# Performance work log

Measured on AMD Instinct MI355X. Metric: run time of the kernel, lower is better.

Reference implementation:

```python
import jax, jax.numpy as jnp
import numpy as np

B, L, E, H, D = 4, 4096, 1024, 16, 64  # batch, seq, embed, heads, head_dim
EPS = 1e-6


def setup_inputs() -> dict:
    key = jax.random.key(0)
    k1, k2, k3 = jax.random.split(key, 3)
    return {
        "q": jax.random.normal(k1, (B, L, E), dtype=jnp.float32),
        "k": jax.random.normal(k2, (B, L, E), dtype=jnp.float32),
        "v": jax.random.normal(k3, (B, L, E), dtype=jnp.float32),
        "mask": jnp.ones((B, L), dtype=jnp.float32),
    }


def _split_heads(x):
    # (B, L, E) -> (B*H, L, D)
    return x.reshape(B, L, H, D).transpose(0, 2, 1, 3).reshape(B * H, L, D)


def reference(q, k, v, mask):
    # feature map: relu
    q = jax.nn.relu(q)
    k = jax.nn.relu(k)
    # padding mask applied to keys/values
    k = k * mask[:, :, None]
    v = v * mask[:, :, None]
    q = _split_heads(q)
    k = _split_heads(k)
    v = _split_heads(v)
    # cosFormer sin/cos reweighting: pi/2 * i / m for i = 1..L
    idx = (np.pi / 2) * jnp.arange(1, L + 1, dtype=jnp.float32) / L
    s = jnp.sin(idx)[None, :, None]  # (1, L, 1)
    c = jnp.cos(idx)[None, :, None]
    q_ = jnp.concatenate([q * s, q * c], axis=-1)  # (B*H, L, 2D)
    k_ = jnp.concatenate([k * s, k * c], axis=-1)
    # linear-attention KV accumulation (non-causal): (B*H, 2D, D)
    kv = jnp.einsum('nld,nlm->ndm', k_, v)
    # normalizer
    z = 1.0 / jnp.maximum(jnp.einsum('nld,nd->nl', q_, k_.sum(axis=1)), EPS)
    out = jnp.einsum('nld,ndm,nl->nlm', q_, kv, z)  # (B*H, L, D)
    return out.reshape(B, H, L, D)
```

## Files before the change

### kernel.cpp

```cpp
#include <hip/hip_runtime.h>
#include <hip/hip_bf16.h>
#include <math.h>

#define B_ 4
#define L_ 4096
#define E_ 1024
#define H_ 16
#define D_ 64
#define N_ 64
#define D2_ 128
#define EPS_ 1e-6f

#define CH_ 16
#define LC_ (L_ / CH_)
#define LT_ 64

typedef short short8 __attribute__((ext_vector_type(8)));
typedef float f32x4 __attribute__((ext_vector_type(4)));
typedef unsigned int u32;
typedef unsigned short u16;

static __device__ __forceinline__ u32 pack2bf(float a, float b) {
  union { __hip_bfloat16 h; u16 s; } x, y;
  x.h = __float2bfloat16(a);
  y.h = __float2bfloat16(b);
  return (u32)x.s | ((u32)y.s << 16);
}

__global__ __launch_bounds__(256, 4) void phase1_mfma(
    const float* __restrict__ k, const float* __restrict__ v,
    const float* __restrict__ mask,
    float* __restrict__ part_kv, float* __restrict__ part_ks) {
  __shared__ __align__(16) u16 ka[D2_ * 72];
  __shared__ __align__(16) u16 vt[D_ * 72];
  __shared__ float msh[LT_], ssh[LT_], csh[LT_];

  const int bid = blockIdx.x;
  const int n = bid & 63;
  const int ch = bid >> 6;
  const int b = n >> 4;
  const int h = n & 15;
  const int t = threadIdx.x;
  const int wv = t >> 6;
  const int lane = t & 63;
  const int c_lo = lane & 15;
  const int lp = lane >> 4;
  const int c = wv * 16 + c_lo;

  f32x4 acc[2][4];
#pragma unroll
  for (int i = 0; i < 2; ++i)
#pragma unroll
    for (int j = 0; j < 4; ++j) acc[i][j] = (f32x4)0.f;
  float kss = 0.f, ksc = 0.f;

  const float angscale = 0.5f * 3.14159265358979f / (float)L_;

  for (int st = 0; st < LC_ / LT_; ++st) {
    const int l0 = ch * LC_ + st * LT_;
    __syncthreads();
    if (t < LT_) {
      const int gl = l0 + t;
      msh[t] = mask[b * L_ + gl];
      const float ang = (float)(gl + 1) * angscale;
      ssh[t] = __sinf(ang);
      csh[t] = __cosf(ang);
    }
    __syncthreads();
#pragma unroll
    for (int i = 0; i < 8; ++i) {
      const int l = 8 * i + 2 * lp;
      const size_t g0 = (size_t)(b * L_ + l0 + l) * E_ + h * 64 + c;
      const float k0 = k[g0], k1 = k[g0 + E_];
      const float v0 = v[g0], v1 = v[g0 + E_];
      const float m0 = msh[l], m1 = msh[l + 1];
      const float s0 = ssh[l], s1 = ssh[l + 1];
      const float c0 = csh[l], c1 = csh[l + 1];
      const float kr0 = fmaxf(k0, 0.f) * m0;
      const float kr1 = fmaxf(k1, 0.f) * m1;
      const float ks0 = kr0 * s0, ks1 = kr1 * s1;
      const float kc0 = kr0 * c0, kc1 = kr1 * c1;
      const int li = l >> 1;
      ((u32*)ka)[c * 36 + li]        = pack2bf(ks0, ks1);
      ((u32*)ka)[(c + 64) * 36 + li] = pack2bf(kc0, kc1);
      ((u32*)vt)[c * 36 + li]        = pack2bf(v0 * m0, v1 * m1);
      kss += ks0 + ks1;
      ksc += kc0 + kc1;
    }
    __syncthreads();
#pragma unroll
    for (int kk = 0; kk < 2; ++kk) {
      const int colo = kk * 32 + lp * 8;
      short8 af[2], bfr[4];
#pragma unroll
      for (int dt = 0; dt < 2; ++dt)
        af[dt] = *(const short8*)&ka[(wv * 32 + dt * 16 + c_lo) * 72 + colo];
#pragma unroll
      for (int mt = 0; mt < 4; ++mt)
        bfr[mt] = *(const short8*)&vt[(mt * 16 + c_lo) * 72 + colo];
#pragma unroll
      for (int dt = 0; dt < 2; ++dt)
#pragma unroll
        for (int mt = 0; mt < 4; ++mt)
          acc[dt][mt] = __builtin_amdgcn_mfma_f32_16x16x32_bf16(
              af[dt], bfr[mt], acc[dt][mt], 0, 0, 0);
    }
  }

  const size_t pbase = (size_t)(ch * N_ + n) * (D2_ * D_);
#pragma unroll
  for (int dt = 0; dt < 2; ++dt) {
    const int d = wv * 32 + dt * 16 + lp * 4;
#pragma unroll
    for (int mt = 0; mt < 4; ++mt) {
      const int mcol = mt * 16 + c_lo;
#pragma unroll
      for (int r = 0; r < 4; ++r)
        part_kv[pbase + (size_t)(d + r) * D_ + mcol] = acc[dt][mt][r];
    }
  }
  kss += __shfl_xor(kss, 16); kss += __shfl_xor(kss, 32);
  ksc += __shfl_xor(ksc, 16); ksc += __shfl_xor(ksc, 32);
  if (lp == 0) {
    part_ks[(size_t)(ch * N_ + n) * D2_ + c] = kss;
    part_ks[(size_t)(ch * N_ + n) * D2_ + c + 64] = ksc;
  }
}

__global__ __launch_bounds__(256) void reduce_t(
    const float* __restrict__ part_kv, const float* __restrict__ part_ks,
    u16* __restrict__ kvt, float* __restrict__ ks) {
  __shared__ float kvsh[D2_ * 65];
  const int n = blockIdx.x;
  const int t = threadIdx.x;

  for (int e = t; e < D2_ * D_; e += 256) {
    float s = 0.f;
#pragma unroll
    for (int cc = 0; cc < CH_; ++cc)
      s += part_kv[(size_t)(cc * N_ + n) * (D2_ * D_) + e];
    kvsh[(e >> 6) * 65 + (e & 63)] = s;
  }
  if (t < D2_) {
    float s = 0.f;
#pragma unroll
    for (int cc = 0; cc < CH_; ++cc)
      s += part_ks[(size_t)(cc * N_ + n) * D2_ + t];
    ks[n * D2_ + t] = s;
  }
  __syncthreads();
  for (int e = t; e < D2_ * D_; e += 256) {
    const int mcol = e >> 7, d = e & 127;
    union { __hip_bfloat16 h; u16 s; } cv;
    cv.h = __float2bfloat16(kvsh[d * 65 + mcol]);
    kvt[(size_t)n * (D2_ * D_) + (size_t)mcol * D2_ + d] = cv.s;
  }
}

__global__ __launch_bounds__(256, 4) void phase2_mfma(
    const float* __restrict__ q, const u16* __restrict__ kvt,
    const float* __restrict__ ks, float* __restrict__ out) {
  __shared__ __align__(16) u16 qa[64 * 136];
  __shared__ __align__(16) u16 kb[64 * 136];
  __shared__ __align__(16) u16 ksb[16 * 136];
  __shared__ float ssh[64], csh[64];

  const int bid = blockIdx.x;
  const int n = bid & 63;
  const int lc = bid >> 6;
  const int b = n >> 4, h = n & 15;
  const int t = threadIdx.x;
  const int wv = t >> 6, lane = t & 63;
  const int c_lo = lane & 15, quad = lane >> 4;
  const int l0 = lc * 64;

  if (t < 64) {
    const int gl = l0 + t;
    const float ang = (float)(gl + 1) * (0.5f * 3.14159265358979f / (float)L_);
    ssh[t] = __sinf(ang);
    csh[t] = __cosf(ang);
  }
  if (t < 68)
    ((u32*)ksb)[t] = (t < 64) ? pack2bf(ks[n * D2_ + 2 * t], ks[n * D2_ + 2 * t + 1]) : 0u;
  for (int i = 68 + t; i < 16 * 68; i += 256) ((u32*)ksb)[i] = 0u;
  {
    const u32* kv32 = (const u32*)(kvt + (size_t)n * (D2_ * D_));
#pragma unroll
    for (int i = 0; i < 16; ++i) {
      const int idx = t + 256 * i;
      ((u32*)kb)[(idx >> 6) * 68 + (idx & 63)] = kv32[idx];
    }
  }
  __syncthreads();

#pragma unroll
  for (int i = 0; i < 16; ++i) {
    const int l = wv + 4 * i;
    const int gl = l0 + l;
    float qv = q[(size_t)(b * L_ + gl) * E_ + h * 64 + lane];
    qv = fmaxf(qv, 0.f);
    const float qs = qv * ssh[l], qc = qv * csh[l];
    union { __hip_bfloat16 h; u16 s; } c1, c2;
    c1.h = __float2bfloat16(qs);
    c2.h = __float2bfloat16(qc);
    qa[l * 136 + lane] = c1.s;
    qa[l * 136 + lane + 64] = c2.s;
  }
  __syncthreads();

  f32x4 acc[4], acc5;
#pragma unroll
  for (int mt = 0; mt < 4; ++mt) acc[mt] = (f32x4)0.f;
  acc5 = (f32x4)0.f;

#pragma unroll
  for (int kk = 0; kk < 4; ++kk) {
    const int colo = kk * 32 + quad * 8;
    const short8 af = *(const short8*)&qa[(wv * 16 + c_lo) * 136 + colo];
#pragma unroll
    for (int mt = 0; mt < 4; ++mt) {
      const short8 bfr = *(const short8*)&kb[(mt * 16 + c_lo) * 136 + colo];
      acc[mt] = __builtin_amdgcn_mfma_f32_16x16x32_bf16(af, bfr, acc[mt], 0, 0, 0);
    }
    const short8 bks = *(const short8*)&ksb[c_lo * 136 + colo];
    acc5 = __builtin_amdgcn_mfma_f32_16x16x32_bf16(af, bks, acc5, 0, 0, 0);
  }

#pragma unroll
  for (int r = 0; r < 4; ++r) {
    const float den = __shfl(acc5[r], quad * 16);
    const float z = 1.f / fmaxf(den, EPS_);
    const int gl = l0 + wv * 16 + quad * 4 + r;
    const size_t ob = (size_t)n * (L_ * D_) + (size_t)gl * D_;
#pragma unroll
    for (int mt = 0; mt < 4; ++mt)
      out[ob + mt * 16 + c_lo] = acc[mt][r] * z;
  }
}

extern "C" void kernel_launch(void* const* d_in, const int* in_sizes, int n_in,
                              void* d_out, int out_size, void* d_ws,
                              size_t ws_size, hipStream_t stream) {
  const float* q = (const float*)d_in[0];
  const float* k = (const float*)d_in[1];
  const float* v = (const float*)d_in[2];
  const float* mask = (const float*)d_in[3];
  float* out = (float*)d_out;

  float* part_kv = (float*)d_ws;
  float* part_ks = part_kv + (size_t)CH_ * N_ * D2_ * D_;
  u16* kvt = (u16*)(part_ks + (size_t)CH_ * N_ * D2_);
  float* ks = (float*)(kvt + (size_t)N_ * D2_ * D_);

  phase1_mfma<<<dim3(CH_ * N_), dim3(256), 0, stream>>>(k, v, mask, part_kv, part_ks);
  reduce_t<<<dim3(N_), dim3(256), 0, stream>>>(part_kv, part_ks, kvt, ks);
  phase2_mfma<<<dim3(N_ * 64), dim3(256), 0, stream>>>(q, kvt, ks, out);
}
```

Measured before the change: 247.1 us.

## Prefetch K/V in registers, split reduction, drop LDS staging in phase2

Phase1 now computes the mask and sin/cos tables for the whole chunk once and software-prefetches the next K/V tile into registers while MFMAs run on the current one. The reduction kernel is split eight ways per head for more parallelism, and it writes a feature-interleaved bf16 KV and a bf16 key-sum vector. Phase2 drops all shared-memory staging: it loads q with float4 loads straight into MFMA operand registers, interleaving sin and cos features to match the new layout, and reads KV fragments directly from global memory. This trades LDS traffic and barriers for more register pressure and uncoalesced global fragment reads that rely on the cache.

```diff
diff --git a/kernel.cpp b/kernel.cpp
--- a/kernel.cpp
+++ b/kernel.cpp
@@ -1,6 +1,5 @@
 #include <hip/hip_runtime.h>
 #include <hip/hip_bf16.h>
-#include <math.h>
 
 #define B_ 4
 #define L_ 4096
@@ -12,19 +11,21 @@
 #define EPS_ 1e-6f
 
 #define CH_ 16
-#define LC_ (L_ / CH_)
-#define LT_ 64
+#define LC_ 256
+#define ANGSC (0.5f * 3.14159265358979f / (float)L_)
 
 typedef short short8 __attribute__((ext_vector_type(8)));
 typedef float f32x4 __attribute__((ext_vector_type(4)));
 typedef unsigned int u32;
 typedef unsigned short u16;
 
+static __device__ __forceinline__ u16 bf16u(float x) {
+  union { __hip_bfloat16 h; u16 s; } u;
+  u.h = __float2bfloat16(x);
+  return u.s;
+}
 static __device__ __forceinline__ u32 pack2bf(float a, float b) {
-  union { __hip_bfloat16 h; u16 s; } x, y;
-  x.h = __float2bfloat16(a);
-  y.h = __float2bfloat16(b);
-  return (u32)x.s | ((u32)y.s << 16);
+  return (u32)bf16u(a) | ((u32)bf16u(b) << 16);
 }
 
 __global__ __launch_bounds__(256, 4) void phase1_mfma(
@@ -33,19 +34,37 @@
     float* __restrict__ part_kv, float* __restrict__ part_ks) {
   __shared__ __align__(16) u16 ka[D2_ * 72];
   __shared__ __align__(16) u16 vt[D_ * 72];
-  __shared__ float msh[LT_], ssh[LT_], csh[LT_];
+  __shared__ float mm[LC_], ms[LC_], mc[LC_];
 
   const int bid = blockIdx.x;
-  const int n = bid & 63;
-  const int ch = bid >> 6;
-  const int b = n >> 4;
-  const int h = n & 15;
+  const int n = bid & 63, ch = bid >> 6;
+  const int b = n >> 4, h = n & 15;
   const int t = threadIdx.x;
-  const int wv = t >> 6;
-  const int lane = t & 63;
-  const int c_lo = lane & 15;
-  const int lp = lane >> 4;
+  const int wv = t >> 6, lane = t & 63;
+  const int c_lo = lane & 15, lp = lane >> 4;
   const int c = wv * 16 + c_lo;
+
+  {
+    const int gl = ch * LC_ + t;
+    const float m = mask[b * L_ + gl];
+    const float ang = (float)(gl + 1) * ANGSC;
+    mm[t] = m;
+    ms[t] = m * __sinf(ang);
+    mc[t] = m * __cosf(ang);
+  }
+
+  const float* kbase = k + (size_t)(b * L_ + ch * LC_) * E_ + h * 64 + c;
+  const float* vbase = v + (size_t)(b * L_ + ch * LC_) * E_ + h * 64 + c;
+
+  float pk0[8], pk1[8], pv0[8], pv1[8];
+#pragma unroll
+  for (int i = 0; i < 8; ++i) {
+    const int l = 8 * i + 2 * lp;
+    pk0[i] = kbase[(size_t)l * E_];
+    pk1[i] = kbase[(size_t)(l + 1) * E_];
+    pv0[i] = vbase[(size_t)l * E_];
+    pv1[i] = vbase[(size_t)(l + 1) * E_];
+  }
 
   f32x4 acc[2][4];
 #pragma unroll
@@ -54,40 +73,32 @@
     for (int j = 0; j < 4; ++j) acc[i][j] = (f32x4)0.f;
   float kss = 0.f, ksc = 0.f;
 
-  const float angscale = 0.5f * 3.14159265358979f / (float)L_;
-
-  for (int st = 0; st < LC_ / LT_; ++st) {
-    const int l0 = ch * LC_ + st * LT_;
+  for (int st = 0; st < 4; ++st) {
     __syncthreads();
-    if (t < LT_) {
-      const int gl = l0 + t;
-      msh[t] = mask[b * L_ + gl];
-      const float ang = (float)(gl + 1) * angscale;
-      ssh[t] = __sinf(ang);
-      csh[t] = __cosf(ang);
+#pragma unroll
+    for (int i = 0; i < 8; ++i) {
+      const int l = 8 * i + 2 * lp, lg = st * 64 + l, li = 4 * i + lp;
+      const float kr0 = fmaxf(pk0[i], 0.f), kr1 = fmaxf(pk1[i], 0.f);
+      const float a0 = kr0 * ms[lg], a1 = kr1 * ms[lg + 1];
+      const float c0 = kr0 * mc[lg], c1 = kr1 * mc[lg + 1];
+      ((u32*)ka)[c * 36 + li] = pack2bf(a0, a1);
+      ((u32*)ka)[(c + 64) * 36 + li] = pack2bf(c0, c1);
+      ((u32*)vt)[c * 36 + li] = pack2bf(pv0[i] * mm[lg], pv1[i] * mm[lg + 1]);
+      kss += a0 + a1;
+      ksc += c0 + c1;
     }
     __syncthreads();
-#pragma unroll
-    for (int i = 0; i < 8; ++i) {
-      const int l = 8 * i + 2 * lp;
-      const size_t g0 = (size_t)(b * L_ + l0 + l) * E_ + h * 64 + c;
-      const float k0 = k[g0], k1 = k[g0 + E_];
-      const float v0 = v[g0], v1 = v[g0 + E_];
-      const float m0 = msh[l], m1 = msh[l + 1];
-      const float s0 = ssh[l], s1 = ssh[l + 1];
-      const float c0 = csh[l], c1 = csh[l + 1];
-      const float kr0 = fmaxf(k0, 0.f) * m0;
-      const float kr1 = fmaxf(k1, 0.f) * m1;
-      const float ks0 = kr0 * s0, ks1 = kr1 * s1;
-      const float kc0 = kr0 * c0, kc1 = kr1 * c1;
-      const int li = l >> 1;
-      ((u32*)ka)[c * 36 + li]        = pack2bf(ks0, ks1);
-      ((u32*)ka)[(c + 64) * 36 + li] = pack2bf(kc0, kc1);
-      ((u32*)vt)[c * 36 + li]        = pack2bf(v0 * m0, v1 * m1);
-      kss += ks0 + ks1;
-      ksc += kc0 + kc1;
-    }
-    __syncthreads();
+    if (st < 3) {
+      const int lo = (st + 1) * 64;
+#pragma unroll
+      for (int i = 0; i < 8; ++i) {
+        const int l = lo + 8 * i + 2 * lp;
+        pk0[i] = kbase[(size_t)l * E_];
+        pk1[i] = kbase[(size_t)(l + 1) * E_];
+        pv0[i] = vbase[(size_t)l * E_];
+        pv1[i] = vbase[(size_t)(l + 1) * E_];
+      }
+    }
 #pragma unroll
     for (int kk = 0; kk < 2; ++kk) {
       const int colo = kk * 32 + lp * 8;
@@ -129,112 +140,95 @@
 
 __global__ __launch_bounds__(256) void reduce_t(
     const float* __restrict__ part_kv, const float* __restrict__ part_ks,
-    u16* __restrict__ kvt, float* __restrict__ ks) {
-  __shared__ float kvsh[D2_ * 65];
-  const int n = blockIdx.x;
+    u16* __restrict__ kvt, u16* __restrict__ ksb) {
+  __shared__ float l0[8][65], l1[8][65];
+  const int n = blockIdx.x & 63, fs = blockIdx.x >> 6;
   const int t = threadIdx.x;
 
-  for (int e = t; e < D2_ * D_; e += 256) {
+#pragma unroll
+  for (int p = 0; p < 4; ++p) {
+    const int idx = t + 256 * p;
+    const int g = idx >> 9, dd = (idx >> 6) & 7, m = idx & 63;
+    const int d = g * 64 + fs * 8 + dd;
     float s = 0.f;
 #pragma unroll
     for (int cc = 0; cc < CH_; ++cc)
-      s += part_kv[(size_t)(cc * N_ + n) * (D2_ * D_) + e];
-    kvsh[(e >> 6) * 65 + (e & 63)] = s;
-  }
-  if (t < D2_) {
+      s += part_kv[(size_t)(cc * N_ + n) * (D2_ * D_) + d * 64 + m];
+    if (g == 0) l0[dd][m] = s; else l1[dd][m] = s;
+  }
+  if (fs == 0 && t < D2_) {
     float s = 0.f;
 #pragma unroll
     for (int cc = 0; cc < CH_; ++cc)
       s += part_ks[(size_t)(cc * N_ + n) * D2_ + t];
-    ks[n * D2_ + t] = s;
+    const int dloc = t & 63, half = t >> 6;
+    ksb[n * D2_ + 2 * dloc + half] = bf16u(s);
   }
   __syncthreads();
-  for (int e = t; e < D2_ * D_; e += 256) {
-    const int mcol = e >> 7, d = e & 127;
-    union { __hip_bfloat16 h; u16 s; } cv;
-    cv.h = __float2bfloat16(kvsh[d * 65 + mcol]);
-    kvt[(size_t)n * (D2_ * D_) + (size_t)mcol * D2_ + d] = cv.s;
+  u32* kvt32 = (u32*)(kvt + (size_t)n * (D_ * D2_));
+#pragma unroll
+  for (int p = 0; p < 2; ++p) {
+    const int idx = t + 256 * p;
+    const int j = idx & 7, m = idx >> 3;
+    kvt32[m * 64 + fs * 8 + j] = pack2bf(l0[j][m], l1[j][m]);
   }
 }
 
 __global__ __launch_bounds__(256, 4) void phase2_mfma(
     const float* __restrict__ q, const u16* __restrict__ kvt,
-    const float* __restrict__ ks, float* __restrict__ out) {
-  __shared__ __align__(16) u16 qa[64 * 136];
-  __shared__ __align__(16) u16 kb[64 * 136];
-  __shared__ __align__(16) u16 ksb[16 * 136];
-  __shared__ float ssh[64], csh[64];
-
+    const u16* __restrict__ ksb, float* __restrict__ out) {
   const int bid = blockIdx.x;
-  const int n = bid & 63;
-  const int lc = bid >> 6;
+  const int n = bid & 63, lt = bid >> 6;
   const int b = n >> 4, h = n & 15;
   const int t = threadIdx.x;
   const int wv = t >> 6, lane = t & 63;
   const int c_lo = lane & 15, quad = lane >> 4;
-  const int l0 = lc * 64;
-
-  if (t < 64) {
-    const int gl = l0 + t;
-    const float ang = (float)(gl + 1) * (0.5f * 3.14159265358979f / (float)L_);
-    ssh[t] = __sinf(ang);
-    csh[t] = __cosf(ang);
-  }
-  if (t < 68)
-    ((u32*)ksb)[t] = (t < 64) ? pack2bf(ks[n * D2_ + 2 * t], ks[n * D2_ + 2 * t + 1]) : 0u;
-  for (int i = 68 + t; i < 16 * 68; i += 256) ((u32*)ksb)[i] = 0u;
-  {
-    const u32* kv32 = (const u32*)(kvt + (size_t)n * (D2_ * D_));
-#pragma unroll
-    for (int i = 0; i < 16; ++i) {
-      const int idx = t + 256 * i;
-      ((u32*)kb)[(idx >> 6) * 68 + (idx & 63)] = kv32[idx];
-    }
-  }
-  __syncthreads();
-
-#pragma unroll
-  for (int i = 0; i < 16; ++i) {
-    const int l = wv + 4 * i;
-    const int gl = l0 + l;
-    float qv = q[(size_t)(b * L_ + gl) * E_ + h * 64 + lane];
-    qv = fmaxf(qv, 0.f);
-    const float qs = qv * ssh[l], qc = qv * csh[l];
-    union { __hip_bfloat16 h; u16 s; } c1, c2;
-    c1.h = __float2bfloat16(qs);
-    c2.h = __float2bfloat16(qc);
-    qa[l * 136 + lane] = c1.s;
-    qa[l * 136 + lane + 64] = c2.s;
-  }
-  __syncthreads();
-
-  f32x4 acc[4], acc5;
+  const int l = lt * 64 + wv * 16 + c_lo;
+
+  const float ang = (float)(l + 1) * ANGSC;
+  const float sn = __sinf(ang), cs = __cosf(ang);
+
+  const float* qrow = q + (size_t)(b * L_ + l) * E_ + h * 64;
+  short8 af[4];
+#pragma unroll
+  for (int kk = 0; kk < 4; ++kk) {
+    const float4 qv = *(const float4*)(qrow + kk * 16 + quad * 4);
+    const float x = fmaxf(qv.x, 0.f), y = fmaxf(qv.y, 0.f);
+    const float z2 = fmaxf(qv.z, 0.f), w = fmaxf(qv.w, 0.f);
+    short8 a;
+    a[0] = (short)bf16u(x * sn); a[1] = (short)bf16u(x * cs);
+    a[2] = (short)bf16u(y * sn); a[3] = (short)bf16u(y * cs);
+    a[4] = (short)bf16u(z2 * sn); a[5] = (short)bf16u(z2 * cs);
+    a[6] = (short)bf16u(w * sn); a[7] = (short)bf16u(w * cs);
+    af[kk] = a;
+  }
+
+  const u16* kvh = kvt + (size_t)n * (D_ * D2_);
+  const u16* ksh = ksb + n * D2_;
+  f32x4 acc[4], acc5 = (f32x4)0.f;
 #pragma unroll
   for (int mt = 0; mt < 4; ++mt) acc[mt] = (f32x4)0.f;
-  acc5 = (f32x4)0.f;
 
 #pragma unroll
   for (int kk = 0; kk < 4; ++kk) {
-    const int colo = kk * 32 + quad * 8;
-    const short8 af = *(const short8*)&qa[(wv * 16 + c_lo) * 136 + colo];
+    const int fo = kk * 32 + quad * 8;
 #pragma unroll
     for (int mt = 0; mt < 4; ++mt) {
-      const short8 bfr = *(const short8*)&kb[(mt * 16 + c_lo) * 136 + colo];
-      acc[mt] = __builtin_amdgcn_mfma_f32_16x16x32_bf16(af, bfr, acc[mt], 0, 0, 0);
-    }
-    const short8 bks = *(const short8*)&ksb[c_lo * 136 + colo];
-    acc5 = __builtin_amdgcn_mfma_f32_16x16x32_bf16(af, bks, acc5, 0, 0, 0);
+      const short8 bfr = *(const short8*)&kvh[(mt * 16 + c_lo) * D2_ + fo];
+      acc[mt] = __builtin_amdgcn_mfma_f32_16x16x32_bf16(af[kk], bfr, acc[mt], 0, 0, 0);
+    }
+    const short8 bks = *(const short8*)&ksh[fo];
+    acc5 = __builtin_amdgcn_mfma_f32_16x16x32_bf16(af[kk], bks, acc5, 0, 0, 0);
   }
 
 #pragma unroll
   for (int r = 0; r < 4; ++r) {
     const float den = __shfl(acc5[r], quad * 16);
-    const float z = 1.f / fmaxf(den, EPS_);
-    const int gl = l0 + wv * 16 + quad * 4 + r;
-    const size_t ob = (size_t)n * (L_ * D_) + (size_t)gl * D_;
-#pragma unroll
-    for (int mt = 0; mt < 4; ++mt)
-      out[ob + mt * 16 + c_lo] = acc[mt][r] * z;
+    const float zz = 1.f / fmaxf(den, EPS_);
+    const int gl = lt * 64 + wv * 16 + quad * 4 + r;
+    float* ob = out + (size_t)n * (L_ * D_) + (size_t)gl * D_;
+#pragma unroll
+    for (int mt = 0; mt < 4; ++mt) ob[mt * 16 + c_lo] = acc[mt][r] * zz;
   }
 }
 
@@ -250,9 +244,9 @@
   float* part_kv = (float*)d_ws;
   float* part_ks = part_kv + (size_t)CH_ * N_ * D2_ * D_;
   u16* kvt = (u16*)(part_ks + (size_t)CH_ * N_ * D2_);
-  float* ks = (float*)(kvt + (size_t)N_ * D2_ * D_);
+  u16* ksb = kvt + (size_t)N_ * D2_ * D_;
 
   phase1_mfma<<<dim3(CH_ * N_), dim3(256), 0, stream>>>(k, v, mask, part_kv, part_ks);
-  reduce_t<<<dim3(N_), dim3(256), 0, stream>>>(part_kv, part_ks, kvt, ks);
-  phase2_mfma<<<dim3(N_ * 64), dim3(256), 0, stream>>>(q, kvt, ks, out);
-}
+  reduce_t<<<dim3(8 * N_), dim3(256), 0, stream>>>(part_kv, part_ks, kvt, ksb);
+  phase2_mfma<<<dim3(N_ * 64), dim3(256), 0, stream>>>(q, kvt, ksb, out);
+}
```

After: 266.1 us. 1.08x slower.
